# Kernel tuning notes

Measured on AMD Instinct MI355X. Metric: run time of the kernel, lower is better.

The kernel has to match this reference:

```python
import jax, jax.numpy as jnp
import numpy as np

B, S, F = 512, 512, 128   # batch, seq_len, facts_size (= querry_size)
H1, H2 = 80, 40
PAD = float(-2**32 + 1)


def setup_inputs() -> dict:
    key = jax.random.key(0)
    ks = jax.random.split(key, 12)
    inp = {
        "query": jax.random.normal(ks[0], (B, F), jnp.float32),
        "facts": jax.random.normal(ks[1], (B, S, F), jnp.float32),
        "mask": jax.random.randint(ks[2], (B, S), 0, 2, jnp.int32),
        # mlp1: querry_size -> facts_size
        "W1": jax.random.normal(ks[3], (F, F), jnp.float32) / np.sqrt(F),
        "b1": jnp.zeros((F,), jnp.float32),
        # PReLU alpha (per-feature, init zeros)
        "alpha": jnp.zeros((F,), jnp.float32),
        # mlp2: 4*F -> 80
        "W2": jax.random.normal(ks[4], (4 * F, H1), jnp.float32) / np.sqrt(4 * F),
        "b2": jnp.zeros((H1,), jnp.float32),
        # mlp3: 80 -> 40
        "W3": jax.random.normal(ks[5], (H1, H2), jnp.float32) / np.sqrt(H1),
        "b3": jnp.zeros((H2,), jnp.float32),
        # mlp4: 40 -> 1
        "W4": jax.random.normal(ks[6], (H2, 1), jnp.float32) / np.sqrt(H2),
        "b4": jnp.zeros((1,), jnp.float32),
    }
    return inp


def reference(query, facts, mask, W1, b1, alpha, W2, b2, W3, b3, W4, b4):
    # mlp1 + PReLU on the query
    q = query @ W1 + b1                                   # [B, F]
    q = jnp.where(q >= 0, q, alpha * q)                   # PReLU, alpha per-feature
    # broadcast query over sequence (tile+reshape in the original)
    qs = jnp.broadcast_to(q[:, None, :], (q.shape[0], S, F))  # [B, S, F]
    din = jnp.concatenate([qs, facts, qs - facts, qs * facts], axis=-1)  # [B,S,4F]
    h1 = jax.nn.sigmoid(din @ W2 + b2)                    # [B, S, 80]
    h2 = jax.nn.sigmoid(h1 @ W3 + b3)                     # [B, S, 40]
    scores = (h2 @ W4 + b4)[..., 0][:, None, :]           # [B, 1, S]
    key_masks = (mask == 1)[:, None, :]                   # [B, 1, S]
    scores = jnp.where(key_masks, scores, PAD)
    scores = jax.nn.softmax(scores, axis=-1)              # softmax over seq
    out = jnp.einsum("bqs,bsf->bqf", scores, facts)       # [B, 1, F]  (mode SUM)
    return out
```

## Files before the change

kernel.cpp:

```cpp
#include <hip/hip_runtime.h>
#include <hip/hip_bf16.h>

typedef __bf16 bf16x8 __attribute__((ext_vector_type(8)));
typedef float  f32x4  __attribute__((ext_vector_type(4)));
typedef float  f32x2  __attribute__((ext_vector_type(2)));

#define WBT_STRIDE 136
#define H1_STRIDE  104
#define W3T_STRIDE 104

__global__ __launch_bounds__(512, 4)
void attn_fused(const float* __restrict__ query,
                const float* __restrict__ facts,
                const int*   __restrict__ mask,
                const float* __restrict__ W1, const float* __restrict__ b1,
                const float* __restrict__ alpha,
                const float* __restrict__ W2, const float* __restrict__ b2,
                const float* __restrict__ W3, const float* __restrict__ b3,
                const float* __restrict__ W4,
                float* __restrict__ out)
{
    __shared__ __align__(16) __bf16 WbT[80 * WBT_STRIDE];
    __shared__ __align__(16) __bf16 W3T[48 * W3T_STRIDE];
    __shared__ __align__(16) __bf16 h1all[128 * H1_STRIDE];
    __shared__ float qy[128], qs[128], qcs[80];
    __shared__ float qpart[4][128], qcp[4][80];
    __shared__ float w4s[48], b3s[48];
    __shared__ float scores[512];
    __shared__ float Zw[8];

    const int b = blockIdx.x, t = threadIdx.x;
    const int wave = t >> 6, lane = t & 63, qd = lane >> 4, m = lane & 15;
    const float* fb = facts + (size_t)b * (512 * 128);
    const int*   mb = mask + b * 512;

    f32x4 av[2][4][2];
    int mv[4];
    {
        const float* p0 = &fb[(size_t)(wave * 64 + m) * 128 + qd * 8];
        #pragma unroll
        for (int kc = 0; kc < 4; ++kc) {
            av[0][kc][0] = *(const f32x4*)(p0 + kc * 32);
            av[0][kc][1] = *(const f32x4*)(p0 + kc * 32 + 4);
        }
        #pragma unroll
        for (int tl = 0; tl < 4; ++tl) mv[tl] = mb[wave * 64 + tl * 16 + m];
    }

    if (t < 128) qy[t] = query[b * 128 + t];
    for (int e = t; e < 48 * 96; e += 512) {
        int j = e / 96, k = e % 96;
        W3T[j * W3T_STRIDE + k] = (j < 40 && k < 80) ? (__bf16)W3[k * 40 + j]
                                                     : (__bf16)0.0f;
    }
    for (int e = t; e < 128 * 16; e += 512) {
        int r = e >> 4, c = 80 + (e & 15);
        h1all[r * H1_STRIDE + c] = (__bf16)0.0f;
    }
    if (t < 48) { w4s[t] = (t < 40) ? W4[t] : 0.f; b3s[t] = (t < 40) ? b3[t] : 0.f; }
    __syncthreads();

    {
        int j = t & 127, kh = t >> 7;
        float acc = (kh == 0) ? b1[j] : 0.f;
        const float* w1p = W1 + (kh * 32) * 128 + j;
        #pragma unroll 8
        for (int k = 0; k < 32; ++k) acc = fmaf(qy[kh * 32 + k], w1p[k * 128], acc);
        qpart[kh][j] = acc;
    }
    __syncthreads();
    if (t < 128) {
        float s = (qpart[0][t] + qpart[1][t]) + (qpart[2][t] + qpart[3][t]);
        qs[t] = (s >= 0.f) ? s : alpha[t] * s;
    }
    __syncthreads();

    if (t < 320) {
        int jj = t % 80, hh = t / 80;
        float acc = (hh == 0) ? b2[jj] : 0.f;
        #pragma unroll 8
        for (int k = hh * 32; k < hh * 32 + 32; ++k)
            acc = fmaf(qs[k], W2[k * 80 + jj] + W2[(256 + k) * 80 + jj], acc);
        qcp[hh][jj] = acc;
    }
    for (int e = t; e < 128 * 80; e += 512) {
        int k = e / 80, n = e - k * 80;
        float w = W2[(128 + k) * 80 + n] - W2[(256 + k) * 80 + n]
                + qs[k] * W2[(384 + k) * 80 + n];
        WbT[n * WBT_STRIDE + k] = (__bf16)w;
    }
    __syncthreads();
    if (t < 80) qcs[t] = (qcp[0][t] + qcp[1][t]) + (qcp[2][t] + qcp[3][t]);
    __syncthreads();

    __bf16* h1w = &h1all[wave * 16 * H1_STRIDE];

    #pragma unroll
    for (int tile = 0; tile < 4; ++tile) {
        const int p = tile & 1;

        if (tile < 3) {
            const float* pn = &fb[(size_t)(wave * 64 + (tile + 1) * 16 + m) * 128 + qd * 8];
            #pragma unroll
            for (int kc = 0; kc < 4; ++kc) {
                av[1 - p][kc][0] = *(const f32x4*)(pn + kc * 32);
                av[1 - p][kc][1] = *(const f32x4*)(pn + kc * 32 + 4);
            }
        }

        bf16x8 af[4];
        #pragma unroll
        for (int kc = 0; kc < 4; ++kc)
            #pragma unroll
            for (int i = 0; i < 8; ++i)
                af[kc][i] = (__bf16)((i < 4) ? av[p][kc][0][i] : av[p][kc][1][i - 4]);

        #pragma unroll
        for (int ct = 0; ct < 5; ++ct) {
            f32x4 acc = {0.f, 0.f, 0.f, 0.f};
            const int n1 = ct * 16 + m;
            #pragma unroll
            for (int kc = 0; kc < 4; ++kc) {
                bf16x8 bfr = *(const bf16x8*)&WbT[n1 * WBT_STRIDE + kc * 32 + qd * 8];
                acc = __builtin_amdgcn_mfma_f32_16x16x32_bf16(af[kc], bfr, acc, 0, 0, 0);
            }
            const float qc = qcs[n1];
            #pragma unroll
            for (int r = 0; r < 4; ++r) {
                float x = acc[r] + qc;
                float h = __builtin_amdgcn_rcpf(1.0f + __expf(-x));
                h1w[(qd * 4 + r) * H1_STRIDE + n1] = (__bf16)h;
            }
        }
        asm volatile("s_waitcnt lgkmcnt(0)" ::: "memory");

        bf16x8 a2[3];
        #pragma unroll
        for (int kc = 0; kc < 3; ++kc)
            a2[kc] = *(const bf16x8*)&h1w[m * H1_STRIDE + kc * 32 + qd * 8];
        float sc[4] = {0.f, 0.f, 0.f, 0.f};
        #pragma unroll
        for (int ct = 0; ct < 3; ++ct) {
            f32x4 acc2 = {0.f, 0.f, 0.f, 0.f};
            #pragma unroll
            for (int kc = 0; kc < 3; ++kc) {
                bf16x8 bfr = *(const bf16x8*)&W3T[(ct * 16 + m) * W3T_STRIDE + kc * 32 + qd * 8];
                acc2 = __builtin_amdgcn_mfma_f32_16x16x32_bf16(a2[kc], bfr, acc2, 0, 0, 0);
            }
            const int col = ct * 16 + m;
            const float w4v = w4s[col], b3v = b3s[col];
            #pragma unroll
            for (int r = 0; r < 4; ++r) {
                float h2 = __builtin_amdgcn_rcpf(1.0f + __expf(-(acc2[r] + b3v)));
                sc[r] = fmaf(h2, w4v, sc[r]);
            }
        }
        #pragma unroll
        for (int d = 1; d < 16; d <<= 1)
            #pragma unroll
            for (int r = 0; r < 4; ++r)
                sc[r] += __shfl_xor(sc[r], d);

        const int idx = ((((m >> 2) << 4) | m) << 2);
        float s0v = __int_as_float(__builtin_amdgcn_ds_bpermute(idx, __float_as_int(sc[0])));
        float s1v = __int_as_float(__builtin_amdgcn_ds_bpermute(idx, __float_as_int(sc[1])));
        float s2v = __int_as_float(__builtin_amdgcn_ds_bpermute(idx, __float_as_int(sc[2])));
        float s3v = __int_as_float(__builtin_amdgcn_ds_bpermute(idx, __float_as_int(sc[3])));
        const int rr = m & 3;
        float srow = (rr == 0) ? s0v : (rr == 1) ? s1v : (rr == 2) ? s2v : s3v;

        const float pm = (mv[tile] == 1) ? __expf(srow) : 0.f;
        if (lane < 16) scores[wave * 64 + tile * 16 + lane] = pm;
    }
    __syncthreads();

    float z = scores[t];
    #pragma unroll
    for (int d = 1; d < 64; d <<= 1) z += __shfl_xor(z, d);
    if (lane == 0) Zw[wave] = z;

    float a0 = 0.f, a1 = 0.f;
    {
        const float* rp = fb + (size_t)(wave * 64) * 128 + 2 * lane;
        const float* pp = &scores[wave * 64];
        #pragma unroll 8
        for (int s = 0; s < 64; ++s) {
            f32x2 v = *(const f32x2*)(rp + (size_t)s * 128);
            const float p = pp[s];
            a0 = fmaf(p, v[0], a0);
            a1 = fmaf(p, v[1], a1);
        }
    }
    float* outw = (float*)h1all;
    __syncthreads();
    outw[wave * 128 + 2 * lane]     = a0;
    outw[wave * 128 + 2 * lane + 1] = a1;
    __syncthreads();

    if (t < 128) {
        float Zg = 0.f, v = 0.f;
        #pragma unroll
        for (int w = 0; w < 8; ++w) { v += outw[w * 128 + t]; Zg += Zw[w]; }
        out[b * 128 + t] = v / Zg;
    }
}

extern "C" void kernel_launch(void* const* d_in, const int* in_sizes, int n_in,
                              void* d_out, int out_size, void* d_ws, size_t ws_size,
                              hipStream_t stream) {
    (void)in_sizes; (void)n_in; (void)d_ws; (void)ws_size; (void)out_size;
    const float* query = (const float*)d_in[0];
    const float* facts = (const float*)d_in[1];
    const int*   mask  = (const int*)d_in[2];
    const float* W1 = (const float*)d_in[3];
    const float* b1 = (const float*)d_in[4];
    const float* al = (const float*)d_in[5];
    const float* W2 = (const float*)d_in[6];
    const float* b2 = (const float*)d_in[7];
    const float* W3 = (const float*)d_in[8];
    const float* b3 = (const float*)d_in[9];
    const float* W4 = (const float*)d_in[10];
    const float* b4 = (const float*)d_in[11];
    (void)b4;
    attn_fused<<<dim3(512), dim3(512), 0, stream>>>(
        query, facts, mask, W1, b1, al, W2, b2, W3, b3, W4, (float*)d_out);
}
```

Measured before the change: 234.2 us.

## Preload all facts tiles as bf16 upfront, use DPP row reductions for scores

All four facts tiles per wave are loaded and converted to bf16 at kernel start instead of double-buffered per tile. This issues every global load before the weight-preparation phase so that their latency overlaps that setup work. The 16-lane score reduction now uses DPP row-rotate adds instead of shuffles, and a single bpermute replaces four after selecting the per-lane value. The final weighted-sum loop unroll also rises from 8 to 16. Holding 16 bf16x8 fragments raises register pressure, which could hurt occupancy under the 512x4 launch bounds.

```diff
diff --git a/kernel.cpp b/kernel.cpp
--- a/kernel.cpp
+++ b/kernel.cpp
@@ -8,6 +8,13 @@
 #define WBT_STRIDE 136
 #define H1_STRIDE  104
 #define W3T_STRIDE 104
+
+template <int CTRL>
+__device__ __forceinline__ float dpp_rotadd(float x) {
+    int xi = __float_as_int(x);
+    int yi = __builtin_amdgcn_update_dpp(xi, xi, CTRL, 0xf, 0xf, false);
+    return x + __int_as_float(yi);
+}
 
 __global__ __launch_bounds__(512, 4)
 void attn_fused(const float* __restrict__ query,
@@ -34,18 +41,26 @@
     const float* fb = facts + (size_t)b * (512 * 128);
     const int*   mb = mask + b * 512;
 
-    f32x4 av[2][4][2];
+    bf16x8 afA[4][4];
     int mv[4];
-    {
-        const float* p0 = &fb[(size_t)(wave * 64 + m) * 128 + qd * 8];
+    #pragma unroll
+    for (int tl = 0; tl < 4; ++tl) {
+        const float* p0 = &fb[(size_t)(wave * 64 + tl * 16 + m) * 128 + qd * 8];
+        f32x4 lo[4], hi[4];
         #pragma unroll
         for (int kc = 0; kc < 4; ++kc) {
-            av[0][kc][0] = *(const f32x4*)(p0 + kc * 32);
-            av[0][kc][1] = *(const f32x4*)(p0 + kc * 32 + 4);
-        }
-        #pragma unroll
-        for (int tl = 0; tl < 4; ++tl) mv[tl] = mb[wave * 64 + tl * 16 + m];
-    }
+            lo[kc] = *(const f32x4*)(p0 + kc * 32);
+            hi[kc] = *(const f32x4*)(p0 + kc * 32 + 4);
+        }
+        #pragma unroll
+        for (int kc = 0; kc < 4; ++kc)
+            #pragma unroll
+            for (int i = 0; i < 8; ++i)
+                afA[tl][kc][i] = (__bf16)((i < 4) ? lo[kc][i] : hi[kc][i - 4]);
+    }
+    #pragma unroll
+    for (int tl = 0; tl < 4; ++tl) mv[tl] = mb[wave * 64 + tl * 16 + m];
+    asm volatile("" ::: "memory");
 
     if (t < 128) qy[t] = query[b * 128 + t];
     for (int e = t; e < 48 * 96; e += 512) {
@@ -97,24 +112,6 @@
 
     #pragma unroll
     for (int tile = 0; tile < 4; ++tile) {
-        const int p = tile & 1;
-
-        if (tile < 3) {
-            const float* pn = &fb[(size_t)(wave * 64 + (tile + 1) * 16 + m) * 128 + qd * 8];
-            #pragma unroll
-            for (int kc = 0; kc < 4; ++kc) {
-                av[1 - p][kc][0] = *(const f32x4*)(pn + kc * 32);
-                av[1 - p][kc][1] = *(const f32x4*)(pn + kc * 32 + 4);
-            }
-        }
-
-        bf16x8 af[4];
-        #pragma unroll
-        for (int kc = 0; kc < 4; ++kc)
-            #pragma unroll
-            for (int i = 0; i < 8; ++i)
-                af[kc][i] = (__bf16)((i < 4) ? av[p][kc][0][i] : av[p][kc][1][i - 4]);
-
         #pragma unroll
         for (int ct = 0; ct < 5; ++ct) {
             f32x4 acc = {0.f, 0.f, 0.f, 0.f};
@@ -122,7 +119,7 @@
             #pragma unroll
             for (int kc = 0; kc < 4; ++kc) {
                 bf16x8 bfr = *(const bf16x8*)&WbT[n1 * WBT_STRIDE + kc * 32 + qd * 8];
-                acc = __builtin_amdgcn_mfma_f32_16x16x32_bf16(af[kc], bfr, acc, 0, 0, 0);
+                acc = __builtin_amdgcn_mfma_f32_16x16x32_bf16(afA[tile][kc], bfr, acc, 0, 0, 0);
             }
             const float qc = qcs[n1];
             #pragma unroll
@@ -156,18 +153,15 @@
             }
         }
         #pragma unroll
-        for (int d = 1; d < 16; d <<= 1)
-            #pragma unroll
-            for (int r = 0; r < 4; ++r)
-                sc[r] += __shfl_xor(sc[r], d);
-
+        for (int r = 0; r < 4; ++r) {
+            sc[r] = dpp_rotadd<0x121>(sc[r]);
+            sc[r] = dpp_rotadd<0x122>(sc[r]);
+            sc[r] = dpp_rotadd<0x124>(sc[r]);
+            sc[r] = dpp_rotadd<0x128>(sc[r]);
+        }
+        float y = (m & 2) ? ((m & 1) ? sc[3] : sc[2]) : ((m & 1) ? sc[1] : sc[0]);
         const int idx = ((((m >> 2) << 4) | m) << 2);
-        float s0v = __int_as_float(__builtin_amdgcn_ds_bpermute(idx, __float_as_int(sc[0])));
-        float s1v = __int_as_float(__builtin_amdgcn_ds_bpermute(idx, __float_as_int(sc[1])));
-        float s2v = __int_as_float(__builtin_amdgcn_ds_bpermute(idx, __float_as_int(sc[2])));
-        float s3v = __int_as_float(__builtin_amdgcn_ds_bpermute(idx, __float_as_int(sc[3])));
-        const int rr = m & 3;
-        float srow = (rr == 0) ? s0v : (rr == 1) ? s1v : (rr == 2) ? s2v : s3v;
+        float srow = __int_as_float(__builtin_amdgcn_ds_bpermute(idx, __float_as_int(y)));
 
         const float pm = (mv[tile] == 1) ? __expf(srow) : 0.f;
         if (lane < 16) scores[wave * 64 + tile * 16 + lane] = pm;
@@ -183,7 +177,7 @@
     {
         const float* rp = fb + (size_t)(wave * 64) * 128 + 2 * lane;
         const float* pp = &scores[wave * 64];
-        #pragma unroll 8
+        #pragma unroll 16
         for (int s = 0; s < 64; ++s) {
             f32x2 v = *(const f32x2*)(rp + (size_t)s * 128);
             const float p = pp[s];
```

New measurement: 296.8 us. 26.7% more time.
